# Performance work log

Hardware: AMD Instinct MI355X
Metric: run time of the kernel (lower is better)

## Reference

```python
import jax, jax.numpy as jnp
import numpy as np

NEG = -1000000.0  # mask value used by the torch module


def setup_inputs() -> dict:
    key = jax.random.key(0)
    kq, kk, kv, kl = jax.random.split(key, 4)
    B, Lq, Lk, d = 16, 2048, 2048, 128
    queries = jax.random.normal(kq, (B, Lq, d), dtype=jnp.float32)
    keys = jax.random.normal(kk, (B, Lk, d), dtype=jnp.float32)
    values = jax.random.normal(kv, (B, Lk, d), dtype=jnp.float32)
    valid_lens = jax.random.randint(kl, (B,), 1, Lk + 1, dtype=jnp.int64)
    return {"queries": queries, "keys": keys, "values": values, "valid_lens": valid_lens}


def reference(queries, keys, values, valid_lens):
    d = queries.shape[-1]
    # scores: [B, Lq, Lk]
    scores = jnp.einsum("bqd,bkd->bqk", queries, keys) / jnp.sqrt(jnp.asarray(d, queries.dtype))
    # valid_lens is [B]; mask key positions >= valid_len (broadcast over query rows)
    Lk = keys.shape[1]
    mask = jnp.arange(Lk)[None, None, :] < valid_lens[:, None, None]  # [B, 1, Lk]
    scores = jnp.where(mask, scores, NEG)
    attn = jax.nn.softmax(scores, axis=-1)
    # dropout p=0.0 -> identity
    return jnp.einsum("bqk,bkd->bqd", attn, values)
```

## Files before the change

kernel.cpp:

```cpp
#include <hip/hip_runtime.h>
#include <hip/hip_fp16.h>


typedef _Float16 f16x2 __attribute__((ext_vector_type(2)));
typedef _Float16 f16x4 __attribute__((ext_vector_type(4)));
typedef _Float16 f16x8 __attribute__((ext_vector_type(8)));
typedef __fp16   n16x2 __attribute__((ext_vector_type(2)));
typedef float    f32x4 __attribute__((ext_vector_type(4)));

#define LQ 2048
#define LK 2048
#define DIM 128
#define KT 64
#define NW 4
#define TILEB 16384
#define BATCHB (32 * TILEB)
#define CFIX 10.0f

__device__ __forceinline__ f16x2 cvt2(float a, float b) {
    n16x2 t = __builtin_amdgcn_cvt_pkrtz(a, b);
    return __builtin_bit_cast(f16x2, t);
}

__device__ __forceinline__ f16x8 pk8(float4 a, float4 b) {
    f16x2 p0 = cvt2(a.x, a.y), p1 = cvt2(a.z, a.w);
    f16x2 p2 = cvt2(b.x, b.y), p3 = cvt2(b.z, b.w);
    f16x8 r;
    r[0]=p0[0]; r[1]=p0[1]; r[2]=p1[0]; r[3]=p1[1];
    r[4]=p2[0]; r[5]=p2[1]; r[6]=p3[0]; r[7]=p3[1];
    return r;
}

__device__ __forceinline__ float fel(const float4& a, const float4& b, int d) {
    const float arr[8] = {a.x,a.y,a.z,a.w,b.x,b.y,b.z,b.w};
    return arr[d];
}

__device__ __forceinline__ int k_off(int r, int dbyte) {
    return ((r << 8) + dbyte) ^ ((r & 7) << 4);
}
__device__ __forceinline__ int vt_off(int d, int k) {
    return d*128 + ((((k >> 3) ^ ((d ^ (d >> 3)) & 7)) << 4) + (k & 7) * 2);
}

__global__ __launch_bounds__(256)
void prep_kernel(const float* __restrict__ K, const float* __restrict__ V,
                 char* __restrict__ Khs, char* __restrict__ Vts) {
    const int blk = blockIdx.x, tid = threadIdx.x;
    if (blk < 512) {
        __shared__ _Float16 t[64 * 136];
        const int b = blk >> 5, kt = blk & 31, k0 = kt * 64;
        const float* src = V + ((size_t)b * LK + k0) * DIM;
        #pragma unroll
        for (int i = 0; i < 4; ++i) {
            int e = i * 2048 + tid * 8;
            int row = e >> 7, d = e & 127;
            float4 a = *(const float4*)(src + row * DIM + d);
            float4 c = *(const float4*)(src + row * DIM + d + 4);
            *(f16x8*)(&t[row * 136 + d]) = pk8(a, c);
        }
        __syncthreads();
        char* out = Vts + (size_t)(b * 32 + kt) * TILEB;
        const int d = tid >> 1, khf = (tid & 1) * 4;
        const int sd = (d ^ (d >> 3)) & 7;
        #pragma unroll
        for (int c = 0; c < 4; ++c) {
            f16x8 w;
            #pragma unroll
            for (int j = 0; j < 8; ++j) w[j] = t[((khf + c) * 8 + j) * 136 + d];
            *(f16x8*)(out + d * 128 + (((khf + c) ^ sd) << 4)) = w;
        }
    } else {
        size_t e = ((size_t)(blk - 512) * 256 + tid) * 8;
        float4 a = *(const float4*)(K + e);
        float4 c = *(const float4*)(K + e + 4);
        size_t krow = e >> 7; int d0 = (int)(e & 127);
        size_t b = krow >> 11; int k = (int)(krow & 2047);
        char* out = Khs + (b * 32 + (k >> 6)) * TILEB;
        int r = k & 63;
        *(f16x8*)(out + k_off(r, d0 << 1)) = pk8(a, c);
    }
}

template<bool WS>
__global__ __launch_bounds__(256, 2)
void fa_kernel(const float* __restrict__ Qg, const float* __restrict__ Kg,
               const float* __restrict__ Vg, const char* __restrict__ Khs,
               const char* __restrict__ Vts, const int* __restrict__ VLg,
               float* __restrict__ Og)
{
    __shared__ __align__(16) char ldsbuf[2][2 * TILEB];
    __shared__ __align__(16) char ldsP[NW][2048];

    const int tid = threadIdx.x, wv = tid >> 6, lane = tid & 63;
    const int lg = lane >> 4, ln = lane & 15;
    const int blk = blockIdx.x;
    const int b = 2 * (blk & 7) + ((blk >> 3) & 1);
    const int q0 = (blk >> 4) * 64 + wv * 16;
    const int nvalid = VLg[b];
    const int nt = (nvalid + KT - 1) >> 6;
    const float SCL = 0.08838834764831845f * 1.44269504088896341f;

    const char*  Khb  = Khs + (size_t)b * BATCHB;
    const char*  Vtb  = Vts + (size_t)b * BATCHB;
    const float* Kb32 = Kg + (size_t)b * LK * DIM;
    const float* Vb32 = Vg + (size_t)b * LK * DIM;

    float4 ka[4], kb4[4], va[4], vb[4];

    auto stage_dma = [&](int buf, int t) {
        const char* ks = Khb + (size_t)t * TILEB + wv * 4096 + lane * 16;
        const char* vs = Vtb + (size_t)t * TILEB + wv * 4096 + lane * 16;
        #pragma unroll
        for (int c = 0; c < 4; ++c) {
            __builtin_amdgcn_global_load_lds(
                (const __attribute__((address_space(1))) unsigned*)(ks + c * 1024),
                (__attribute__((address_space(3))) unsigned*)&ldsbuf[buf][wv * 4096 + c * 1024],
                16, 0, 0);
            __builtin_amdgcn_global_load_lds(
                (const __attribute__((address_space(1))) unsigned*)(vs + c * 1024),
                (__attribute__((address_space(3))) unsigned*)&ldsbuf[buf][TILEB + wv * 4096 + c * 1024],
                16, 0, 0);
        }
    };

    auto issue_fp32 = [&](int k0) {
        #pragma unroll
        for (int i = 0; i < 4; ++i) {
            int c = tid + i*256, row = c >> 4, d0 = (c & 15) * 8;
            const float* s = Kb32 + (size_t)(k0 + row)*DIM + d0;
            ka[i] = *(const float4*)s;  kb4[i] = *(const float4*)(s+4);
        }
        int kq = tid >> 4, d0 = (tid & 15) * 8;
        #pragma unroll
        for (int j = 0; j < 4; ++j) {
            const float* s = Vb32 + (size_t)(k0 + kq*4 + j)*DIM + d0;
            va[j] = *(const float4*)s;  vb[j] = *(const float4*)(s+4);
        }
    };

    auto swrite_fp32 = [&](int buf) {
        char* kb = &ldsbuf[buf][0];
        char* vb2 = &ldsbuf[buf][TILEB];
        #pragma unroll
        for (int i = 0; i < 4; ++i) {
            int c = tid + i*256, row = c >> 4, d0 = (c & 15) * 8;
            *(f16x8*)(kb + k_off(row, d0 << 1)) = pk8(ka[i], kb4[i]);
        }
        int kq = tid >> 4, d0 = (tid & 15) * 8;
        #pragma unroll
        for (int dd = 0; dd < 8; ++dd) {
            f16x2 lo = cvt2(fel(va[0],vb[0],dd), fel(va[1],vb[1],dd));
            f16x2 hi = cvt2(fel(va[2],vb[2],dd), fel(va[3],vb[3],dd));
            f16x4 w; w[0]=lo[0]; w[1]=lo[1]; w[2]=hi[0]; w[3]=hi[1];
            *(f16x4*)(vb2 + vt_off(d0 + dd, 4*kq)) = w;
        }
    };

    if constexpr (WS) stage_dma(0, 0);
    else              issue_fp32(0);

    f16x8 qf[4];
    {
        const float* qr = Qg + ((size_t)b*LQ + q0 + ln)*DIM + lg*8;
        #pragma unroll
        for (int dc = 0; dc < 4; ++dc) {
            float4 a = *(const float4*)(qr + dc*32);
            float4 c = *(const float4*)(qr + dc*32 + 4);
            a.x*=SCL; a.y*=SCL; a.z*=SCL; a.w*=SCL;
            c.x*=SCL; c.y*=SCL; c.z*=SCL; c.w*=SCL;
            qf[dc] = pk8(a, c);
        }
    }

    if constexpr (!WS) swrite_fp32(0);
    __syncthreads();

    f32x4 acc[8];
    #pragma unroll
    for (int t = 0; t < 8; ++t) acc[t] = (f32x4){0.f,0.f,0.f,0.f};
    float lrow = 0.f;

    char* pbase = &ldsP[wv][0];
    int cur = 0;

    for (int t = 0; t < nt; ++t) {
        const int k0 = t * KT;
        const bool more = (t + 1 < nt);
        if (more) {
            if constexpr (WS) stage_dma(cur ^ 1, t + 1);
            else              issue_fp32(k0 + KT);
        }
        char* kbase = &ldsbuf[cur][0];
        char* vbase = &ldsbuf[cur][TILEB];

        f32x4 s[4];
        #pragma unroll
        for (int kc = 0; kc < 4; ++kc) s[kc] = (f32x4){0.f,0.f,0.f,0.f};
        __builtin_amdgcn_s_setprio(1);
        #pragma unroll
        for (int kc = 0; kc < 4; ++kc) {
            #pragma unroll
            for (int dc = 0; dc < 4; ++dc) {
                f16x8 kf = *(const f16x8*)(kbase + k_off(kc*16 + ln, dc*64 + lg*16));
                s[kc] = __builtin_amdgcn_mfma_f32_16x16x32_f16(kf, qf[dc], s[kc], 0,0,0);
            }
        }
        __builtin_amdgcn_s_setprio(0);

        if (k0 + KT > nvalid) {
            #pragma unroll
            for (int kc = 0; kc < 4; ++kc)
                #pragma unroll
                for (int r = 0; r < 4; ++r)
                    if (k0 + kc*16 + 4*lg + r >= nvalid) s[kc][r] = -1e30f;
        }

        float rs = 0.f;
        #pragma unroll
        for (int kc = 0; kc < 4; ++kc) {
            float p0 = __builtin_amdgcn_exp2f(s[kc][0] - CFIX);
            float p1 = __builtin_amdgcn_exp2f(s[kc][1] - CFIX);
            float p2 = __builtin_amdgcn_exp2f(s[kc][2] - CFIX);
            float p3 = __builtin_amdgcn_exp2f(s[kc][3] - CFIX);
            rs += (p0 + p1) + (p2 + p3);
            f16x2 lo = cvt2(p0, p1);
            f16x2 hi = cvt2(p2, p3);
            f16x4 w; w[0]=lo[0]; w[1]=lo[1]; w[2]=hi[0]; w[3]=hi[1];
            *(f16x4*)(pbase + (ln << 7) + ((kc*32 + lg*8) ^ ((ln & 7) << 4))) = w;
        }
        lrow += rs;

        asm volatile("s_waitcnt lgkmcnt(0)" ::: "memory");

        f16x8 af[2];
        #pragma unroll
        for (int kc2 = 0; kc2 < 2; ++kc2)
            af[kc2] = *(const f16x8*)(pbase + (ln << 7) + ((kc2*64 + lg*16) ^ ((ln & 7) << 4)));
        __builtin_amdgcn_s_setprio(1);
        #pragma unroll
        for (int tt = 0; tt < 8; ++tt) {
            #pragma unroll
            for (int kc2 = 0; kc2 < 2; ++kc2) {
                f16x8 bf = *(const f16x8*)(vbase + vt_off(tt*16 + ln, kc2*32 + lg*8));
                acc[tt] = __builtin_amdgcn_mfma_f32_16x16x32_f16(af[kc2], bf, acc[tt], 0,0,0);
            }
        }
        __builtin_amdgcn_s_setprio(0);

        if (more) {
            if constexpr (!WS) swrite_fp32(cur ^ 1);
            __syncthreads();
            cur ^= 1;
        }
    }

    lrow += __shfl_xor(lrow, 16);
    lrow += __shfl_xor(lrow, 32);
    float linv = 1.f / lrow;
    #pragma unroll
    for (int r = 0; r < 4; ++r) {
        float lr = __shfl(linv, 4*lg + r);
        float* orow = Og + ((size_t)b*LQ + q0 + 4*lg + r)*DIM + ln;
        #pragma unroll
        for (int tt = 0; tt < 8; ++tt) orow[tt*16] = acc[tt][r] * lr;
    }
}

extern "C" void kernel_launch(void* const* d_in, const int* in_sizes, int n_in,
                              void* d_out, int out_size, void* d_ws, size_t ws_size,
                              hipStream_t stream) {
    const float* Q  = (const float*)d_in[0];
    const float* K  = (const float*)d_in[1];
    const float* V  = (const float*)d_in[2];
    const int*   VL = (const int*)d_in[3];
    float* O = (float*)d_out;

    const size_t need = (size_t)16 * BATCHB * 2;
    if (ws_size >= need) {
        char* Khs = (char*)d_ws;
        char* Vts = Khs + (size_t)16 * BATCHB;
        prep_kernel<<<dim3(512 + 2048), dim3(256), 0, stream>>>(K, V, Khs, Vts);
        fa_kernel<true><<<dim3(512), dim3(256), 0, stream>>>(Q, K, V, Khs, Vts, VL, O);
    } else {
        fa_kernel<false><<<dim3(512), dim3(256), 0, stream>>>(Q, K, V, nullptr, nullptr, VL, O);
    }
}
```

Before: 66.75 us.

## Preformat K/V into MFMA fragment order and split key tiles across waves

The prep stage now writes K and V in fp16, laid out exactly as the lanes of the 32x32x16 MFMA expect their fragments, and is split into two kernels. The attention kernel then loads K and V fragments straight from global memory into registers with no LDS staging and no block barrier in the loop. Each wave handles 32 queries, and the two wave pairs take alternating key tiles, merging their partial outputs and row sums through LDS at the end. The P operand is rebuilt with cross-lane shuffles instead of an LDS round trip. In exchange, each wave re-reads K/V tiles from global or cache without software prefetch, and register pressure rises.

```diff
diff --git a/kernel.cpp b/kernel.cpp
--- a/kernel.cpp
+++ b/kernel.cpp
@@ -7,12 +7,13 @@
 typedef _Float16 f16x8 __attribute__((ext_vector_type(8)));
 typedef __fp16   n16x2 __attribute__((ext_vector_type(2)));
 typedef float    f32x4 __attribute__((ext_vector_type(4)));
+typedef float    f32x16 __attribute__((ext_vector_type(16)));
+typedef unsigned int  u32;
+typedef unsigned int  u32x4 __attribute__((ext_vector_type(4)));
 
 #define LQ 2048
 #define LK 2048
 #define DIM 128
-#define KT 64
-#define NW 4
 #define TILEB 16384
 #define BATCHB (32 * TILEB)
 #define CFIX 10.0f
@@ -20,6 +21,9 @@
 __device__ __forceinline__ f16x2 cvt2(float a, float b) {
     n16x2 t = __builtin_amdgcn_cvt_pkrtz(a, b);
     return __builtin_bit_cast(f16x2, t);
+}
+__device__ __forceinline__ u32 cvt2u(float a, float b) {
+    return __builtin_bit_cast(u32, __builtin_amdgcn_cvt_pkrtz(a, b));
 }
 
 __device__ __forceinline__ f16x8 pk8(float4 a, float4 b) {
@@ -31,100 +35,226 @@
     return r;
 }
 
+__global__ __launch_bounds__(256)
+void prepK_kernel(const float* __restrict__ K, char* __restrict__ Kf) {
+    size_t e = ((size_t)blockIdx.x * 256 + threadIdx.x) * 8;
+    float4 a = *(const float4*)(K + e);
+    float4 c = *(const float4*)(K + e + 4);
+    size_t krow = e >> 7; int d0 = (int)(e & 127);
+    size_t b = krow >> 11; int k = (int)(krow & 2047);
+    int t = k >> 6, g = (k >> 5) & 1, lo = k & 31;
+    int u = d0 >> 3, dc = u >> 1, hi = u & 1;
+    char* out = Kf + ((b * 32 + t) * 16 + g * 8 + dc) * 1024 + (hi * 32 + lo) * 16;
+    *(f16x8*)out = pk8(a, c);
+}
+
+__global__ __launch_bounds__(256)
+void prepV_kernel(const float* __restrict__ V, char* __restrict__ Vf) {
+    __shared__ _Float16 tl[64 * 136];
+    const int blk = blockIdx.x, tid = threadIdx.x;
+    const int b = blk >> 5, t = blk & 31, k0g = t * 64;
+    const float* src = V + ((size_t)b * LK + k0g) * DIM;
+    #pragma unroll
+    for (int i = 0; i < 4; ++i) {
+        int e = i * 2048 + tid * 8;
+        int row = e >> 7, d = e & 127;
+        float4 a = *(const float4*)(src + row * DIM + d);
+        float4 c = *(const float4*)(src + row * DIM + d + 4);
+        *(f16x8*)(&tl[row * 136 + d]) = pk8(a, c);
+    }
+    __syncthreads();
+    char* out = Vf + (size_t)(b * 32 + t) * TILEB;
+    #pragma unroll
+    for (int c = 0; c < 4; ++c) {
+        int chunk = tid * 4 + c;
+        int f2 = chunk >> 6, l = chunk & 63;
+        int ks = f2 >> 2, dc2 = f2 & 3;
+        int k0 = ks * 16 + (l >> 5) * 8;
+        int d  = dc2 * 32 + (l & 31);
+        f16x8 w;
+        #pragma unroll
+        for (int j = 0; j < 8; ++j) w[j] = tl[(k0 + j) * 136 + d];
+        *(f16x8*)(out + f2 * 1024 + l * 16) = w;
+    }
+}
+
+__global__ __launch_bounds__(256, 2)
+void fa_kernel(const float* __restrict__ Qg, const char* __restrict__ Kf,
+               const char* __restrict__ Vf, const int* __restrict__ VLg,
+               float* __restrict__ Og)
+{
+    __shared__ float scr_o[2][32 * 128];
+    __shared__ float scr_l[2][32];
+
+    const int tid = threadIdx.x, wv = tid >> 6, lane = tid & 63;
+    const int lo = lane & 31, hi = lane >> 5;
+    const int qh = wv & 1, kh = wv >> 1;
+    const int blk = blockIdx.x;
+    const int b = 2 * (blk & 7) + ((blk >> 3) & 1);
+    const int q0 = (blk >> 4) * 64 + qh * 32;
+    const int nvalid = VLg[b];
+    const int nt = (nvalid + 63) >> 6;
+    const float SCL = 0.08838834764831845f * 1.44269504088896341f;
+
+    const char* Kfb = Kf + (size_t)b * BATCHB;
+    const char* Vfb = Vf + (size_t)b * BATCHB;
+
+    f16x8 qf[8];
+    {
+        const float* qr = Qg + ((size_t)b*LQ + q0 + lo)*DIM + hi*8;
+        #pragma unroll
+        for (int dc = 0; dc < 8; ++dc) {
+            float4 a = *(const float4*)(qr + dc*16);
+            float4 c = *(const float4*)(qr + dc*16 + 4);
+            a.x*=SCL; a.y*=SCL; a.z*=SCL; a.w*=SCL;
+            c.x*=SCL; c.y*=SCL; c.z*=SCL; c.w*=SCL;
+            qf[dc] = pk8(a, c);
+        }
+    }
+
+    f32x16 oacc[4];
+    #pragma unroll
+    for (int d = 0; d < 4; ++d)
+        #pragma unroll
+        for (int r = 0; r < 16; ++r) oacc[d][r] = 0.f;
+    float lrow = 0.f;
+
+    for (int t = kh; t < nt; t += 2) {
+        const char* kp = Kfb + (size_t)t * TILEB + lane * 16;
+        const char* vp = Vfb + (size_t)t * TILEB + lane * 16;
+
+        f16x8 kf0[8], kf1[8];
+        #pragma unroll
+        for (int dc = 0; dc < 8; ++dc) kf0[dc] = *(const f16x8*)(kp + dc * 1024);
+        #pragma unroll
+        for (int dc = 0; dc < 8; ++dc) kf1[dc] = *(const f16x8*)(kp + (8 + dc) * 1024);
+        f16x8 vf[16];
+        #pragma unroll
+        for (int f2 = 0; f2 < 16; ++f2) vf[f2] = *(const f16x8*)(vp + f2 * 1024);
+
+        f32x16 s0, s1;
+        #pragma unroll
+        for (int r = 0; r < 16; ++r) { s0[r] = 0.f; s1[r] = 0.f; }
+        __builtin_amdgcn_s_setprio(1);
+        #pragma unroll
+        for (int dc = 0; dc < 8; ++dc) {
+            s0 = __builtin_amdgcn_mfma_f32_32x32x16_f16(kf0[dc], qf[dc], s0, 0, 0, 0);
+            s1 = __builtin_amdgcn_mfma_f32_32x32x16_f16(kf1[dc], qf[dc], s1, 0, 0, 0);
+        }
+        __builtin_amdgcn_s_setprio(0);
+
+        if ((t + 1) * 64 > nvalid) {
+            const int k0 = t * 64;
+            #pragma unroll
+            for (int r = 0; r < 16; ++r) {
+                int key = k0 + (r & 3) + 8 * (r >> 2) + 4 * hi;
+                if (key      >= nvalid) s0[r] = -1e30f;
+                if (key + 32 >= nvalid) s1[r] = -1e30f;
+            }
+        }
+
+        u32 c0[8], c1[8];
+        float rs = 0.f;
+        #pragma unroll
+        for (int m = 0; m < 8; ++m) {
+            float a0 = __builtin_amdgcn_exp2f(s0[2*m]   - CFIX);
+            float a1 = __builtin_amdgcn_exp2f(s0[2*m+1] - CFIX);
+            float b0 = __builtin_amdgcn_exp2f(s1[2*m]   - CFIX);
+            float b1 = __builtin_amdgcn_exp2f(s1[2*m+1] - CFIX);
+            rs += (a0 + a1) + (b0 + b1);
+            c0[m] = cvt2u(a0, a1);
+            c1[m] = cvt2u(b0, b1);
+        }
+        lrow += rs;
+
+        u32 w0[8], w1[8];
+        #pragma unroll
+        for (int m = 0; m < 8; ++m) {
+            w0[m] = __shfl_xor(c0[m], 32);
+            w1[m] = __shfl_xor(c1[m], 32);
+        }
+        f16x8 pa00 = __builtin_bit_cast(f16x8, hi ? (u32x4){w0[2],w0[3],c0[2],c0[3]}
+                                                  : (u32x4){c0[0],c0[1],w0[0],w0[1]});
+        f16x8 pa01 = __builtin_bit_cast(f16x8, hi ? (u32x4){w0[6],w0[7],c0[6],c0[7]}
+                                                  : (u32x4){c0[4],c0[5],w0[4],w0[5]});
+        f16x8 pa10 = __builtin_bit_cast(f16x8, hi ? (u32x4){w1[2],w1[3],c1[2],c1[3]}
+                                                  : (u32x4){c1[0],c1[1],w1[0],w1[1]});
+        f16x8 pa11 = __builtin_bit_cast(f16x8, hi ? (u32x4){w1[6],w1[7],c1[6],c1[7]}
+                                                  : (u32x4){c1[4],c1[5],w1[4],w1[5]});
+
+        __builtin_amdgcn_s_setprio(1);
+        #pragma unroll
+        for (int dc2 = 0; dc2 < 4; ++dc2) {
+            oacc[dc2] = __builtin_amdgcn_mfma_f32_32x32x16_f16(pa00, vf[ 0 + dc2], oacc[dc2], 0,0,0);
+            oacc[dc2] = __builtin_amdgcn_mfma_f32_32x32x16_f16(pa01, vf[ 4 + dc2], oacc[dc2], 0,0,0);
+            oacc[dc2] = __builtin_amdgcn_mfma_f32_32x32x16_f16(pa10, vf[ 8 + dc2], oacc[dc2], 0,0,0);
+            oacc[dc2] = __builtin_amdgcn_mfma_f32_32x32x16_f16(pa11, vf[12 + dc2], oacc[dc2], 0,0,0);
+        }
+        __builtin_amdgcn_s_setprio(0);
+    }
+
+    lrow += __shfl_xor(lrow, 32);
+
+    if (kh == 1) {
+        float* so = &scr_o[qh][0];
+        #pragma unroll
+        for (int r = 0; r < 16; ++r) {
+            int qr = (r & 3) + 8 * (r >> 2) + 4 * hi;
+            #pragma unroll
+            for (int dc2 = 0; dc2 < 4; ++dc2)
+                so[qr * 128 + dc2 * 32 + lo] = oacc[dc2][r];
+        }
+        if (hi == 0) scr_l[qh][lo] = lrow;
+    }
+    __syncthreads();
+    if (kh == 0) {
+        const float* so = &scr_o[qh][0];
+        float lt = lrow + scr_l[qh][lo];
+        float linv = 1.f / lt;
+        #pragma unroll
+        for (int r = 0; r < 16; ++r) {
+            int qr = (r & 3) + 8 * (r >> 2) + 4 * hi;
+            float lv = __shfl(linv, qr);
+            float* orow = Og + ((size_t)b*LQ + q0 + qr)*DIM + lo;
+            #pragma unroll
+            for (int dc2 = 0; dc2 < 4; ++dc2)
+                orow[dc2*32] = (oacc[dc2][r] + so[qr * 128 + dc2 * 32 + lo]) * lv;
+        }
+    }
+}
+
+typedef _Float16 f16x4_t __attribute__((ext_vector_type(4)));
 __device__ __forceinline__ float fel(const float4& a, const float4& b, int d) {
     const float arr[8] = {a.x,a.y,a.z,a.w,b.x,b.y,b.z,b.w};
     return arr[d];
 }
-
-__device__ __forceinline__ int k_off(int r, int dbyte) {
+__device__ __forceinline__ int kfo(int r, int dbyte) {
     return ((r << 8) + dbyte) ^ ((r & 7) << 4);
 }
-__device__ __forceinline__ int vt_off(int d, int k) {
+__device__ __forceinline__ int vto(int d, int k) {
     return d*128 + ((((k >> 3) ^ ((d ^ (d >> 3)) & 7)) << 4) + (k & 7) * 2);
 }
 
-__global__ __launch_bounds__(256)
-void prep_kernel(const float* __restrict__ K, const float* __restrict__ V,
-                 char* __restrict__ Khs, char* __restrict__ Vts) {
-    const int blk = blockIdx.x, tid = threadIdx.x;
-    if (blk < 512) {
-        __shared__ _Float16 t[64 * 136];
-        const int b = blk >> 5, kt = blk & 31, k0 = kt * 64;
-        const float* src = V + ((size_t)b * LK + k0) * DIM;
-        #pragma unroll
-        for (int i = 0; i < 4; ++i) {
-            int e = i * 2048 + tid * 8;
-            int row = e >> 7, d = e & 127;
-            float4 a = *(const float4*)(src + row * DIM + d);
-            float4 c = *(const float4*)(src + row * DIM + d + 4);
-            *(f16x8*)(&t[row * 136 + d]) = pk8(a, c);
-        }
-        __syncthreads();
-        char* out = Vts + (size_t)(b * 32 + kt) * TILEB;
-        const int d = tid >> 1, khf = (tid & 1) * 4;
-        const int sd = (d ^ (d >> 3)) & 7;
-        #pragma unroll
-        for (int c = 0; c < 4; ++c) {
-            f16x8 w;
-            #pragma unroll
-            for (int j = 0; j < 8; ++j) w[j] = t[((khf + c) * 8 + j) * 136 + d];
-            *(f16x8*)(out + d * 128 + (((khf + c) ^ sd) << 4)) = w;
-        }
-    } else {
-        size_t e = ((size_t)(blk - 512) * 256 + tid) * 8;
-        float4 a = *(const float4*)(K + e);
-        float4 c = *(const float4*)(K + e + 4);
-        size_t krow = e >> 7; int d0 = (int)(e & 127);
-        size_t b = krow >> 11; int k = (int)(krow & 2047);
-        char* out = Khs + (b * 32 + (k >> 6)) * TILEB;
-        int r = k & 63;
-        *(f16x8*)(out + k_off(r, d0 << 1)) = pk8(a, c);
-    }
-}
-
-template<bool WS>
 __global__ __launch_bounds__(256, 2)
-void fa_kernel(const float* __restrict__ Qg, const float* __restrict__ Kg,
-               const float* __restrict__ Vg, const char* __restrict__ Khs,
-               const char* __restrict__ Vts, const int* __restrict__ VLg,
-               float* __restrict__ Og)
+void fa_fb(const float* __restrict__ Qg, const float* __restrict__ Kg,
+           const float* __restrict__ Vg, const int* __restrict__ VLg,
+           float* __restrict__ Og)
 {
-    __shared__ __align__(16) char ldsbuf[2][2 * TILEB];
-    __shared__ __align__(16) char ldsP[NW][2048];
-
+    __shared__ __align__(16) char ldsbuf[2][32768];
+    __shared__ __align__(16) char ldsP[4][2048];
     const int tid = threadIdx.x, wv = tid >> 6, lane = tid & 63;
     const int lg = lane >> 4, ln = lane & 15;
     const int blk = blockIdx.x;
     const int b = 2 * (blk & 7) + ((blk >> 3) & 1);
     const int q0 = (blk >> 4) * 64 + wv * 16;
     const int nvalid = VLg[b];
-    const int nt = (nvalid + KT - 1) >> 6;
+    const int nt = (nvalid + 63) >> 6;
     const float SCL = 0.08838834764831845f * 1.44269504088896341f;
-
-    const char*  Khb  = Khs + (size_t)b * BATCHB;
-    const char*  Vtb  = Vts + (size_t)b * BATCHB;
     const float* Kb32 = Kg + (size_t)b * LK * DIM;
     const float* Vb32 = Vg + (size_t)b * LK * DIM;
-
     float4 ka[4], kb4[4], va[4], vb[4];
-
-    auto stage_dma = [&](int buf, int t) {
-        const char* ks = Khb + (size_t)t * TILEB + wv * 4096 + lane * 16;
-        const char* vs = Vtb + (size_t)t * TILEB + wv * 4096 + lane * 16;
-        #pragma unroll
-        for (int c = 0; c < 4; ++c) {
-            __builtin_amdgcn_global_load_lds(
-                (const __attribute__((address_space(1))) unsigned*)(ks + c * 1024),
-                (__attribute__((address_space(3))) unsigned*)&ldsbuf[buf][wv * 4096 + c * 1024],
-                16, 0, 0);
-            __builtin_amdgcn_global_load_lds(
-                (const __attribute__((address_space(1))) unsigned*)(vs + c * 1024),
-                (__attribute__((address_space(3))) unsigned*)&ldsbuf[buf][TILEB + wv * 4096 + c * 1024],
-                16, 0, 0);
-        }
-    };
-
-    auto issue_fp32 = [&](int k0) {
+    auto issue = [&](int t) {
+        int k0 = t * 64;
         #pragma unroll
         for (int i = 0; i < 4; ++i) {
             int c = tid + i*256, row = c >> 4, d0 = (c & 15) * 8;
@@ -138,28 +268,24 @@
             va[j] = *(const float4*)s;  vb[j] = *(const float4*)(s+4);
         }
     };
-
-    auto swrite_fp32 = [&](int buf) {
+    auto swr = [&](int buf) {
         char* kb = &ldsbuf[buf][0];
-        char* vb2 = &ldsbuf[buf][TILEB];
+        char* vb2 = &ldsbuf[buf][16384];
         #pragma unroll
         for (int i = 0; i < 4; ++i) {
             int c = tid + i*256, row = c >> 4, d0 = (c & 15) * 8;
-            *(f16x8*)(kb + k_off(row, d0 << 1)) = pk8(ka[i], kb4[i]);
+            *(f16x8*)(kb + kfo(row, d0 << 1)) = pk8(ka[i], kb4[i]);
         }
         int kq = tid >> 4, d0 = (tid & 15) * 8;
         #pragma unroll
         for (int dd = 0; dd < 8; ++dd) {
-            f16x2 lo = cvt2(fel(va[0],vb[0],dd), fel(va[1],vb[1],dd));
-            f16x2 hi = cvt2(fel(va[2],vb[2],dd), fel(va[3],vb[3],dd));
-            f16x4 w; w[0]=lo[0]; w[1]=lo[1]; w[2]=hi[0]; w[3]=hi[1];
-            *(f16x4*)(vb2 + vt_off(d0 + dd, 4*kq)) = w;
+            f16x2 lw = cvt2(fel(va[0],vb[0],dd), fel(va[1],vb[1],dd));
+            f16x2 hw = cvt2(fel(va[2],vb[2],dd), fel(va[3],vb[3],dd));
+            f16x4_t w; w[0]=lw[0]; w[1]=lw[1]; w[2]=hw[0]; w[3]=hw[1];
+            *(f16x4_t*)(vb2 + vto(d0 + dd, 4*kq)) = w;
         }
     };
-
-    if constexpr (WS) stage_dma(0, 0);
-    else              issue_fp32(0);
-
+    issue(0);
     f16x8 qf[4];
     {
         const float* qr = Qg + ((size_t)b*LQ + q0 + ln)*DIM + lg*8;
@@ -172,50 +298,37 @@
             qf[dc] = pk8(a, c);
         }
     }
-
-    if constexpr (!WS) swrite_fp32(0);
+    swr(0);
     __syncthreads();
-
     f32x4 acc[8];
     #pragma unroll
     for (int t = 0; t < 8; ++t) acc[t] = (f32x4){0.f,0.f,0.f,0.f};
     float lrow = 0.f;
-
     char* pbase = &ldsP[wv][0];
     int cur = 0;
-
     for (int t = 0; t < nt; ++t) {
-        const int k0 = t * KT;
+        const int k0 = t * 64;
         const bool more = (t + 1 < nt);
-        if (more) {
-            if constexpr (WS) stage_dma(cur ^ 1, t + 1);
-            else              issue_fp32(k0 + KT);
-        }
+        if (more) issue(t + 1);
         char* kbase = &ldsbuf[cur][0];
-        char* vbase = &ldsbuf[cur][TILEB];
-
+        char* vbase = &ldsbuf[cur][16384];
         f32x4 s[4];
         #pragma unroll
         for (int kc = 0; kc < 4; ++kc) s[kc] = (f32x4){0.f,0.f,0.f,0.f};
-        __builtin_amdgcn_s_setprio(1);
-        #pragma unroll
-        for (int kc = 0; kc < 4; ++kc) {
+        #pragma unroll
+        for (int kc = 0; kc < 4; ++kc)
             #pragma unroll
             for (int dc = 0; dc < 4; ++dc) {
-                f16x8 kf = *(const f16x8*)(kbase + k_off(kc*16 + ln, dc*64 + lg*16));
+                f16x8 kf = *(const f16x8*)(kbase + kfo(kc*16 + ln, dc*64 + lg*16));
                 s[kc] = __builtin_amdgcn_mfma_f32_16x16x32_f16(kf, qf[dc], s[kc], 0,0,0);
             }
-        }
-        __builtin_amdgcn_s_setprio(0);
-
-        if (k0 + KT > nvalid) {
+        if (k0 + 64 > nvalid) {
             #pragma unroll
             for (int kc = 0; kc < 4; ++kc)
                 #pragma unroll
                 for (int r = 0; r < 4; ++r)
                     if (k0 + kc*16 + 4*lg + r >= nvalid) s[kc][r] = -1e30f;
         }
-
         float rs = 0.f;
         #pragma unroll
         for (int kc = 0; kc < 4; ++kc) {
@@ -224,37 +337,26 @@
             float p2 = __builtin_amdgcn_exp2f(s[kc][2] - CFIX);
             float p3 = __builtin_amdgcn_exp2f(s[kc][3] - CFIX);
             rs += (p0 + p1) + (p2 + p3);
-            f16x2 lo = cvt2(p0, p1);
-            f16x2 hi = cvt2(p2, p3);
-            f16x4 w; w[0]=lo[0]; w[1]=lo[1]; w[2]=hi[0]; w[3]=hi[1];
-            *(f16x4*)(pbase + (ln << 7) + ((kc*32 + lg*8) ^ ((ln & 7) << 4))) = w;
+            f16x2 plo = cvt2(p0, p1);
+            f16x2 phi = cvt2(p2, p3);
+            f16x4_t w; w[0]=plo[0]; w[1]=plo[1]; w[2]=phi[0]; w[3]=phi[1];
+            *(f16x4_t*)(pbase + (ln << 7) + ((kc*32 + lg*8) ^ ((ln & 7) << 4))) = w;
         }
         lrow += rs;
-
         asm volatile("s_waitcnt lgkmcnt(0)" ::: "memory");
-
         f16x8 af[2];
         #pragma unroll
         for (int kc2 = 0; kc2 < 2; ++kc2)
             af[kc2] = *(const f16x8*)(pbase + (ln << 7) + ((kc2*64 + lg*16) ^ ((ln & 7) << 4)));
-        __builtin_amdgcn_s_setprio(1);
-        #pragma unroll
-        for (int tt = 0; tt < 8; ++tt) {
+        #pragma unroll
+        for (int tt = 0; tt < 8; ++tt)
             #pragma unroll
             for (int kc2 = 0; kc2 < 2; ++kc2) {
-                f16x8 bf = *(const f16x8*)(vbase + vt_off(tt*16 + ln, kc2*32 + lg*8));
+                f16x8 bf = *(const f16x8*)(vbase + vto(tt*16 + ln, kc2*32 + lg*8));
                 acc[tt] = __builtin_amdgcn_mfma_f32_16x16x32_f16(af[kc2], bf, acc[tt], 0,0,0);
             }
-        }
-        __builtin_amdgcn_s_setprio(0);
-
-        if (more) {
-            if constexpr (!WS) swrite_fp32(cur ^ 1);
-            __syncthreads();
-            cur ^= 1;
-        }
-    }
-
+        if (more) { swr(cur ^ 1); __syncthreads(); cur ^= 1; }
+    }
     lrow += __shfl_xor(lrow, 16);
     lrow += __shfl_xor(lrow, 32);
     float linv = 1.f / lrow;
@@ -278,11 +380,12 @@
 
     const size_t need = (size_t)16 * BATCHB * 2;
     if (ws_size >= need) {
-        char* Khs = (char*)d_ws;
-        char* Vts = Khs + (size_t)16 * BATCHB;
-        prep_kernel<<<dim3(512 + 2048), dim3(256), 0, stream>>>(K, V, Khs, Vts);
-        fa_kernel<true><<<dim3(512), dim3(256), 0, stream>>>(Q, K, V, Khs, Vts, VL, O);
+        char* Kf = (char*)d_ws;
+        char* Vf = Kf + (size_t)16 * BATCHB;
+        prepK_kernel<<<dim3(2048), dim3(256), 0, stream>>>(K, Kf);
+        prepV_kernel<<<dim3(512),  dim3(256), 0, stream>>>(V, Vf);
+        fa_kernel<<<dim3(512), dim3(256), 0, stream>>>(Q, Kf, Vf, VL, O);
     } else {
-        fa_kernel<false><<<dim3(512), dim3(256), 0, stream>>>(Q, K, V, nullptr, nullptr, VL, O);
-    }
-}
+        fa_fb<<<dim3(512), dim3(256), 0, stream>>>(Q, K, V, VL, O);
+    }
+}
```

Result: slower. 76.47 us (+14.6%).
